# Kernel tuning notes

Measured on AMD Instinct MI355X. Metric: run time of the kernel, lower is better.

Reference implementation:

```python
import jax, jax.numpy as jnp
import numpy as np

D = 1024      # model_dim
H = 2048      # expert hidden_dim
E = 8         # num routed experts
S = 1         # num shared experts
M = 4         # num modes (1 shared expert per mode)
TOP_K = 2
B, L = 2, 2048


def _ffn(x, w1, b1, w2, b2):
    # x: [T, D]; w1: [..., D, H]; stacked experts via einsum
    h = jnp.einsum('td,edh->teh', x, w1) + b1          # [T, E*, H]
    h = jax.nn.gelu(h)
    return jnp.einsum('teh,ehd->ted', h, w2) + b2      # [T, E*, D]


def setup_inputs() -> dict:
    key = jax.random.key(0)
    ks = jax.random.split(key, 16)
    s = 0.02
    inp = {
        'hidden': jax.random.normal(ks[0], (B, L, D), dtype=jnp.float32),
        'mode_ids': jax.random.randint(ks[1], (B, L), 0, M),
        'router_w': jax.random.normal(ks[2], (D, E), dtype=jnp.float32) * s,
        'router_b': jnp.zeros((E,), dtype=jnp.float32),
        'shared_w1': jax.random.normal(ks[3], (S, D, H), dtype=jnp.float32) * s,
        'shared_b1': jnp.zeros((S, H), dtype=jnp.float32),
        'shared_w2': jax.random.normal(ks[4], (S, H, D), dtype=jnp.float32) * s,
        'shared_b2': jnp.zeros((S, D), dtype=jnp.float32),
        'mode_w1': jax.random.normal(ks[5], (M, D, H), dtype=jnp.float32) * s,
        'mode_b1': jnp.zeros((M, H), dtype=jnp.float32),
        'mode_w2': jax.random.normal(ks[6], (M, H, D), dtype=jnp.float32) * s,
        'mode_b2': jnp.zeros((M, D), dtype=jnp.float32),
        'routed_w1': jax.random.normal(ks[7], (E, D, H), dtype=jnp.float32) * s,
        'routed_b1': jnp.zeros((E, H), dtype=jnp.float32),
        'routed_w2': jax.random.normal(ks[8], (E, H, D), dtype=jnp.float32) * s,
        'routed_b2': jnp.zeros((E, D), dtype=jnp.float32),
    }
    return inp


def reference(hidden, mode_ids, router_w, router_b,
              shared_w1, shared_b1, shared_w2, shared_b2,
              mode_w1, mode_b1, mode_w2, mode_b2,
              routed_w1, routed_b1, routed_w2, routed_b2):
    b, l, d = hidden.shape
    flat = hidden.reshape(b * l, d)                         # [T, D]

    # --- router ---
    router_logits = flat @ router_w + router_b              # [T, E]
    router_probs = jax.nn.softmax(router_logits, axis=-1)
    topk_probs, topk_indices = jax.lax.top_k(router_probs, TOP_K)  # [T, K]

    # --- shared experts (mean over S experts) ---
    shared_out = _ffn(flat, shared_w1, shared_b1, shared_w2, shared_b2).mean(axis=1)  # [T, D]

    # --- mode-conditioned shared experts (1 expert per mode) ---
    mode_flat = mode_ids.reshape(-1)                        # [T]
    mode_onehot = jax.nn.one_hot(mode_flat, M, dtype=flat.dtype)   # [T, M]
    mode_all = _ffn(flat, mode_w1, mode_b1, mode_w2, mode_b2)      # [T, M, D]
    mode_out = jnp.einsum('tm,tmd->td', mode_onehot, mode_all)
    shared_out = shared_out + mode_out

    # --- routed experts: combine weights per (token, expert) ---
    # w[t,e] = sum_k topk_probs[t,k] * (topk_indices[t,k] == e)
    combine_w = jnp.einsum('tke,tk->te',
                           jax.nn.one_hot(topk_indices, E, dtype=flat.dtype),
                           topk_probs)                      # [T, E]
    routed_all = _ffn(flat, routed_w1, routed_b1, routed_w2, routed_b2)  # [T, E, D]
    mixed = jnp.einsum('te,ted->td', combine_w, routed_all)

    output = (shared_out + mixed).reshape(b, l, d)
    aux_logits = router_logits.reshape(b, l, E)
    aux_idx = topk_indices.reshape(b, l, TOP_K)
    aux_probs = topk_probs.reshape(b, l, TOP_K)
    return output, aux_logits, aux_idx, aux_probs
```

## Files before the change

kernel.cpp:

```cpp
#include <hip/hip_runtime.h>
#include <hip/hip_bf16.h>

typedef __hip_bfloat16 bf16t;
using f32x4 = __attribute__((ext_vector_type(4))) float;
using s16x8 = __attribute__((ext_vector_type(8))) short;

#define NTOK 4096
#define DIM 1024
#define HID 2048
#define NEXP 8
#define NMODE 4
#define NGRP 13
#define SLOTS_PAD 16640
#define MAXT 144

static constexpr size_t SZ_WT    = (size_t)NGRP * HID * DIM * 2;
static constexpr size_t OFF_WT1  = 0;
static constexpr size_t OFF_OBUF = 0;
static constexpr size_t OFF_WT2  = OFF_WT1 + SZ_WT;
static constexpr size_t OFF_HBUF = OFF_WT2 + SZ_WT;
static constexpr size_t SZ_HBUF  = (size_t)SLOTS_PAD * HID * 2;
static constexpr size_t OFF_XBF  = OFF_HBUF + SZ_HBUF;
static constexpr size_t SZ_XBF   = (size_t)NTOK * DIM * 2;
static constexpr size_t OFF_B1   = OFF_XBF + SZ_XBF;
static constexpr size_t OFF_B2   = OFF_B1 + (size_t)NGRP * HID * 4;
static constexpr size_t OFF_TP   = OFF_B2 + (size_t)NGRP * DIM * 4;
static constexpr size_t OFF_TI   = OFF_TP + (size_t)NTOK * 2 * 4;
static constexpr size_t OFF_MS   = OFF_TI + (size_t)NTOK * 2 * 4;
static constexpr size_t OFF_R0S  = OFF_MS + (size_t)NTOK * 4;
static constexpr size_t OFF_R1S  = OFF_R0S + (size_t)NTOK * 4;
static constexpr size_t OFF_LIST = OFF_R1S + (size_t)NTOK * 4;
static constexpr size_t OFF_TC   = OFF_LIST + (size_t)SLOTS_PAD * 4;
static constexpr size_t OFF_TD   = OFF_TC + 16;
static constexpr size_t WS_NEED  = OFF_TD + (size_t)MAXT * 16;

static __device__ __forceinline__ short fb(float f) {
    bf16t h = __float2bfloat16(f);
    short s; __builtin_memcpy(&s, &h, 2); return s;
}
static __device__ __forceinline__ float bf2f(short s) {
    unsigned u = ((unsigned)(unsigned short)s) << 16;
    float f; __builtin_memcpy(&f, &u, 4); return f;
}

static __device__ __forceinline__ float fast_exp(float x) {
#if __has_builtin(__builtin_amdgcn_exp2f)
    return __builtin_amdgcn_exp2f(x * 1.4426950408889634f);
#else
    return exp2f(x * 1.4426950408889634f);
#endif
}
static __device__ __forceinline__ float fast_rcp(float x) {
#if __has_builtin(__builtin_amdgcn_rcpf)
    return __builtin_amdgcn_rcpf(x);
#else
    return 1.0f / x;
#endif
}
static __device__ __forceinline__ float gelu_tanh(float x) {
    float x2 = x * x;
    float u = 0.7978845608028654f * fmaf(0.044715f * x2, x, x);
    u = fminf(u, 15.0f);
    float t = fast_exp(2.0f * u);
    return x * t * fast_rcp(t + 1.0f);
}

typedef __attribute__((address_space(3))) void lds_void;
typedef const __attribute__((address_space(1))) void gbl_void;
static __device__ __forceinline__ void gload16(const void* g, void* l) {
    __builtin_amdgcn_global_load_lds((gbl_void*)g, (lds_void*)l, 16, 0, 0);
}

struct TPtr {
    const float* s_w1; const float* s_w2;
    const float* m_w1; const float* m_w2;
    const float* r_w1; const float* r_w2;
};

static __device__ __forceinline__ void transpose_tile(
    const float* __restrict__ src, bf16t* __restrict__ dst, int R, int C, int x, int y,
    float (*lds)[64][65], int t) {
    const int c0 = x * 64;
    const int ar = t >> 4, ac = (t & 15) * 4;
    const int bc = t >> 3;
    const int rg = (t & 7) * 8;
#pragma unroll
    for (int it = 0; it < 2; ++it) {
        const int r0 = (y * 2 + it) * 64;
#pragma unroll
        for (int p = 0; p < 4; p++) {
            const int r = p * 16 + ar;
            const float4 v = *(const float4*)(src + (size_t)(r0 + r) * C + (c0 + ac));
            lds[it][r][ac] = v.x; lds[it][r][ac + 1] = v.y;
            lds[it][r][ac + 2] = v.z; lds[it][r][ac + 3] = v.w;
        }
    }
    __syncthreads();
#pragma unroll
    for (int it = 0; it < 2; ++it) {
        const int r0 = (y * 2 + it) * 64;
#pragma unroll
        for (int j = 0; j < 2; j++) {
            const int c = j * 32 + bc;
            unsigned w[4];
#pragma unroll
            for (int u = 0; u < 4; u++) {
                unsigned lo = (unsigned short)fb(lds[it][rg + 2 * u][c]);
                unsigned hi = (unsigned short)fb(lds[it][rg + 2 * u + 1][c]);
                w[u] = (hi << 16) | lo;
            }
            *(uint4*)((char*)dst + ((size_t)(c0 + c) * R + (r0 + rg)) * 2) = make_uint4(w[0], w[1], w[2], w[3]);
        }
    }
}

#define TGRID1 3328
#define RGRID  4352
#define PGRID  4456

__global__ __launch_bounds__(256) void prep_k(
    TPtr tp, bf16t* __restrict__ wt1,
    const float* __restrict__ hidden, const int* __restrict__ mode_ids,
    const float* __restrict__ rw, const float* __restrict__ rb,
    float* __restrict__ aux_logits, float* __restrict__ aux_idx, float* __restrict__ aux_probs,
    float* __restrict__ topk_p, int* __restrict__ topk_i, bf16t* __restrict__ xbf,
    const float* __restrict__ sb1, const float* __restrict__ mb1, const float* __restrict__ rb1,
    const float* __restrict__ sb2, const float* __restrict__ mb2, const float* __restrict__ rb2,
    float* __restrict__ B1c, float* __restrict__ B2c) {
    const int bid = blockIdx.x;
    const int t = threadIdx.x;

    if (bid < TGRID1) {
        __shared__ float lds[2][64][65];
        const size_t MSZ = (size_t)DIM * HID;
        const int z = bid >> 8, rem = bid & 255;
        const int x = (rem >> 3) & 31, y = rem & 7;
        const float* src;
        if (z == 0)      src = tp.s_w1;
        else if (z < 5)  src = tp.m_w1 + (size_t)(z - 1) * MSZ;
        else             src = tp.r_w1 + (size_t)(z - 5) * MSZ;
        transpose_tile(src, wt1 + (size_t)z * MSZ, DIM, HID, x, y, lds, t);
        return;
    }

    if (bid < RGRID) {
        const int tok = (bid - TGRID1) * 4 + (t >> 6);
        const int lane = t & 63;
        const float* x = hidden + (size_t)tok * DIM;
        float acc[NEXP];
#pragma unroll
        for (int e = 0; e < NEXP; e++) acc[e] = 0.f;
#pragma unroll
        for (int i = 0; i < DIM / 64; i++) {
            int d = i * 64 + lane;
            float xv = x[d];
            xbf[(size_t)tok * DIM + d] = __float2bfloat16(xv);
            const float4* w = (const float4*)(rw + (size_t)d * NEXP);
            float4 w0 = w[0], w1 = w[1];
            acc[0] += xv * w0.x; acc[1] += xv * w0.y; acc[2] += xv * w0.z; acc[3] += xv * w0.w;
            acc[4] += xv * w1.x; acc[5] += xv * w1.y; acc[6] += xv * w1.z; acc[7] += xv * w1.w;
        }
#pragma unroll
        for (int off = 32; off >= 1; off >>= 1) {
#pragma unroll
            for (int e = 0; e < NEXP; e++) acc[e] += __shfl_down(acc[e], off, 64);
        }
        if (lane == 0) {
            float lg[NEXP], pb[NEXP];
            float mx = -1e30f;
#pragma unroll
            for (int e = 0; e < NEXP; e++) { lg[e] = acc[e] + rb[e]; mx = fmaxf(mx, lg[e]); }
            float s = 0.f;
#pragma unroll
            for (int e = 0; e < NEXP; e++) { pb[e] = expf(lg[e] - mx); s += pb[e]; }
            float inv = 1.f / s;
#pragma unroll
            for (int e = 0; e < NEXP; e++) { pb[e] *= inv; aux_logits[(size_t)tok * NEXP + e] = lg[e]; }
            int i1 = 0;
            for (int e = 1; e < NEXP; e++) if (pb[e] > pb[i1]) i1 = e;
            int i2 = (i1 == 0) ? 1 : 0;
            for (int e = 0; e < NEXP; e++) { if (e == i1) continue; if (pb[e] > pb[i2]) i2 = e; }
            aux_idx[tok * 2] = (float)i1;  aux_idx[tok * 2 + 1] = (float)i2;
            aux_probs[tok * 2] = pb[i1];   aux_probs[tok * 2 + 1] = pb[i2];
            topk_p[tok * 2] = pb[i1];      topk_p[tok * 2 + 1] = pb[i2];
            topk_i[tok * 2] = i1;          topk_i[tok * 2 + 1] = i2;
        }
        return;
    }

    {
        const int i = (bid - RGRID) * 256 + t;
        if (i < NGRP * HID) {
            int g = i / HID, h = i % HID;
            B1c[i] = (g == 0) ? sb1[h] : (g < 5) ? mb1[(g - 1) * HID + h] : rb1[(g - 5) * HID + h];
        }
        if (i < NGRP * DIM) {
            int g = i / DIM, d = i % DIM;
            B2c[i] = (g == 0) ? sb2[d] : (g < 5) ? mb2[(g - 1) * DIM + d] : rb2[(g - 5) * DIM + d];
        }
    }
}

__global__ __launch_bounds__(1024) void groupfill_k(
    const int* __restrict__ mode_ids, const int* __restrict__ topki,
    int4* __restrict__ tdesc, int* __restrict__ tcount,
    int* __restrict__ list,
    int* __restrict__ ms, int* __restrict__ r0s, int* __restrict__ r1s) {
    __shared__ int cnts[12];
    __shared__ int curs[12];
    const int lane = threadIdx.x & 63;
    const int wave = threadIdx.x >> 6;
    if (threadIdx.x < 12) cnts[threadIdx.x] = 0;
    if (threadIdx.x < SLOTS_PAD - 16384) list[16384 + threadIdx.x] = 0;
    __syncthreads();

    int local[12];
#pragma unroll
    for (int i = 0; i < 12; i++) local[i] = 0;
#pragma unroll
    for (int c = wave; c < NTOK / 64; c += 16) {
        const int t = c * 64 + lane;
        const int m  = mode_ids[t];
        const int e0 = topki[t * 2];
        const int e1 = topki[t * 2 + 1];
#pragma unroll
        for (int b = 0; b < 4; b++) local[b] += __popcll(__ballot(m == b));
#pragma unroll
        for (int b = 0; b < 8; b++) {
            local[4 + b] += __popcll(__ballot(e0 == b));
            local[4 + b] += __popcll(__ballot(e1 == b));
        }
    }
    if (lane == 0) {
#pragma unroll
        for (int i = 0; i < 12; i++) if (local[i]) atomicAdd(&cnts[i], local[i]);
    }
    __syncthreads();

    if (threadIdx.x == 0) {
        int nt = 0;
        auto emit = [&](int off, int c, int g) {
            for (int r0 = 0; r0 < c; r0 += 128) tdesc[nt++] = make_int4(off + r0, min(128, c - r0), g, 0);
        };
        emit(0, NTOK, 0);
        int off = NTOK;
        for (int m = 0; m < NMODE; m++) { curs[m] = off; emit(off, cnts[m], 1 + m); off += cnts[m]; }
        off = 2 * NTOK;
        for (int e = 0; e < NEXP; e++) { curs[NMODE + e] = off; emit(off, cnts[NMODE + e], 5 + e); off += cnts[NMODE + e]; }
        tcount[0] = nt;
    }
    __syncthreads();

    auto put = [&](int bin, bool pred, int payload, int* inv, int t) {
        unsigned long long msk = __ballot(pred);
        if (msk == 0ull) return;
        int leader = __ffsll((unsigned long long)msk) - 1;
        int base = 0;
        if (lane == leader) base = atomicAdd(&curs[bin], __popcll(msk));
        base = __shfl(base, leader, 64);
        if (pred) {
            int pos = base + __popcll(msk & ((1ull << lane) - 1ull));
            list[pos] = payload;
            inv[t] = pos;
        }
    };
#pragma unroll
    for (int it = 0; it < 4; ++it) {
        const int t = it * 1024 + threadIdx.x;
        list[t] = t << 1;
        const int m  = mode_ids[t];
        const int e0 = topki[t * 2], e1 = topki[t * 2 + 1];
#pragma unroll
        for (int b = 0; b < NMODE; b++) put(b, m == b, t << 1, ms, t);
#pragma unroll
        for (int b = 0; b < NEXP; b++) put(NMODE + b, e0 == b, t << 1, r0s, t);
#pragma unroll
        for (int b = 0; b < NEXP; b++) put(NMODE + b, e1 == b, (t << 1) | 1, r1s, t);
    }
}

#define W2GRID 3328
template <int STAGE>
__global__ __launch_bounds__(256, 3) void ffn_gemm_k(
    const bf16t* __restrict__ xbf,
    const bf16t* __restrict__ hbuf,
    const bf16t* __restrict__ wt,
    const float* __restrict__ bias,
    bf16t* __restrict__ obuf,
    const int* __restrict__ list,
    const int4* __restrict__ tdesc,
    const int* __restrict__ tcount,
    const float* __restrict__ w2s, const float* __restrict__ w2m, const float* __restrict__ w2r,
    bf16t* __restrict__ wt2o) {
    constexpr int K   = (STAGE == 1) ? DIM : HID;
    constexpr int N   = (STAGE == 1) ? HID : DIM;
    constexpr int NK  = K / 32;
    constexpr int NTN = N / 128;
    constexpr int NWG = NTN * MAXT;

    __shared__ alignas(16) char smem[49152];

    if constexpr (STAGE == 1) {
        if (blockIdx.x >= NWG) {
            const int id2 = blockIdx.x - NWG;
            const size_t MSZ = (size_t)DIM * HID;
            const int z = id2 >> 8, rem = id2 & 255;
            const int x = rem >> 4, y = rem & 15;
            const float* src;
            if (z == 0)      src = w2s;
            else if (z < 5)  src = w2m + (size_t)(z - 1) * MSZ;
            else             src = w2r + (size_t)(z - 5) * MSZ;
            transpose_tile(src, wt2o + (size_t)z * MSZ, HID, DIM, x, y,
                           (float (*)[64][65])smem, threadIdx.x);
            return;
        }
    }

    char* As = smem;
    char* Bs = smem + 24576;

    const int lin = blockIdx.x;
    const int wg  = (lin & 7) * (NWG >> 3) + (lin >> 3);
    const int ntile = wg / MAXT;
    const int tix = wg - ntile * MAXT;
    if (tix >= tcount[0]) return;
    const int4 td = tdesc[tix];
    const int slot0 = td.x, rows = td.y, gidx = td.z;
    const int n0 = ntile * 128;

    const int tid  = threadIdx.x;
    const int lane = tid & 63;
    const int w    = tid >> 6;
    const int wm   = w >> 1, wn = w & 1;

    const bf16t* wbase = wt + (size_t)gidx * ((size_t)K * N);
    const bf16t* aP[2];
    const bf16t* bP[2];
#pragma unroll
    for (int h = 0; h < 2; h++) {
        const int r  = (w * 2 + h) * 16 + (lane >> 2);
        const int ce = (((lane & 3) ^ ((r >> 1) & 3)) << 3);
        if (STAGE == 1) aP[h] = xbf + (size_t)(list[slot0 + r] >> 1) * DIM + ce;
        else            aP[h] = hbuf + (size_t)(slot0 + r) * HID + ce;
        bP[h] = wbase + (size_t)(n0 + r) * K + ce;
    }

    auto stage = [&](int t) {
        char* la = As + (t % 3) * 8192 + (w * 2) * 1024 + lane * 16;
        char* lb = Bs + (t % 3) * 8192 + (w * 2) * 1024 + lane * 16;
        gload16(aP[0] + t * 32, la);
        gload16(aP[1] + t * 32, la + 1024);
        gload16(bP[0] + t * 32, lb);
        gload16(bP[1] + t * 32, lb + 1024);
    };

    f32x4 acc[4][4];
    const f32x4 zero = {0.f, 0.f, 0.f, 0.f};
#pragma unroll
    for (int i = 0; i < 4; i++)
#pragma unroll
        for (int j = 0; j < 4; j++) acc[i][j] = zero;

    const int lm = lane & 15;
    const int kc = lane >> 4;

    stage(0); stage(1);

    for (int t = 0; t < NK; ++t) {
        const int cur = t % 3;
        if (t + 1 < NK) asm volatile("s_waitcnt vmcnt(4)" ::: "memory");
        else            asm volatile("s_waitcnt vmcnt(0)" ::: "memory");
        __builtin_amdgcn_s_barrier();

        s16x8 av[4], bv[4];
#pragma unroll
        for (int i = 0; i < 4; i++) {
            const int Ra = wm * 64 + i * 16 + lm;
            av[i] = *(const s16x8*)(As + cur * 8192 + Ra * 64 + ((kc ^ ((Ra >> 1) & 3)) << 4));
            const int Rb = wn * 64 + i * 16 + lm;
            bv[i] = *(const s16x8*)(Bs + cur * 8192 + Rb * 64 + ((kc ^ ((Rb >> 1) & 3)) << 4));
        }
        if (t + 2 < NK) stage(t + 2);

        __builtin_amdgcn_s_setprio(1);
#pragma unroll
        for (int mi = 0; mi < 4; mi++)
#pragma unroll
            for (int ni = 0; ni < 4; ni++)
                acc[mi][ni] = __builtin_amdgcn_mfma_f32_16x16x32_bf16(av[mi], bv[ni], acc[mi][ni], 0, 0, 0);
        __builtin_amdgcn_s_setprio(0);
    }

    const int lr = lane >> 4, lc = lane & 15;
#pragma unroll
    for (int ni = 0; ni < 4; ni++) {
        const int col = n0 + wn * 64 + ni * 16 + lc;
        const float bvv = bias[gidx * N + col];
#pragma unroll
        for (int mi = 0; mi < 4; mi++) {
#pragma unroll
            for (int r = 0; r < 4; r++) {
                const int row = wm * 64 + mi * 16 + lr * 4 + r;
                if (row < rows) {
                    float v = acc[mi][ni][r] + bvv;
                    if (STAGE == 1) v = gelu_tanh(v);
                    obuf[(size_t)(slot0 + row) * N + col] = __float2bfloat16(v);
                }
            }
        }
    }
}

__global__ void reduce_k(const bf16t* __restrict__ ob,
                         const int* __restrict__ ms, const int* __restrict__ r0s, const int* __restrict__ r1s,
                         const float* __restrict__ topkp, float* __restrict__ out) {
    const int t = blockIdx.x * 4 + (threadIdx.x >> 7);
    const int d = (threadIdx.x & 127) * 8;
    const s16x8 a = *(const s16x8*)(ob + (size_t)t * DIM + d);
    const s16x8 b = *(const s16x8*)(ob + (size_t)ms[t] * DIM + d);
    const s16x8 c = *(const s16x8*)(ob + (size_t)r0s[t] * DIM + d);
    const s16x8 e = *(const s16x8*)(ob + (size_t)r1s[t] * DIM + d);
    const float p0 = topkp[t * 2], p1 = topkp[t * 2 + 1];
    float o[8];
#pragma unroll
    for (int j = 0; j < 8; j++)
        o[j] = bf2f(a[j]) + bf2f(b[j]) + p0 * bf2f(c[j]) + p1 * bf2f(e[j]);
    float* dst = out + (size_t)t * DIM + d;
    *(float4*)dst = make_float4(o[0], o[1], o[2], o[3]);
    *(float4*)(dst + 4) = make_float4(o[4], o[5], o[6], o[7]);
}

extern "C" void kernel_launch(void* const* d_in, const int* in_sizes, int n_in,
                              void* d_out, int out_size, void* d_ws, size_t ws_size,
                              hipStream_t stream) {
    (void)in_sizes; (void)n_in; (void)out_size;
    if (ws_size < WS_NEED) return;

    const float* hidden   = (const float*)d_in[0];
    const int*   mode_ids = (const int*)d_in[1];
    const float* router_w = (const float*)d_in[2];
    const float* router_b = (const float*)d_in[3];
    TPtr tp;
    tp.s_w1 = (const float*)d_in[4];
    const float* s_b1 = (const float*)d_in[5];
    tp.s_w2 = (const float*)d_in[6];
    const float* s_b2 = (const float*)d_in[7];
    tp.m_w1 = (const float*)d_in[8];
    const float* m_b1 = (const float*)d_in[9];
    tp.m_w2 = (const float*)d_in[10];
    const float* m_b2 = (const float*)d_in[11];
    tp.r_w1 = (const float*)d_in[12];
    const float* r_b1 = (const float*)d_in[13];
    tp.r_w2 = (const float*)d_in[14];
    const float* r_b2 = (const float*)d_in[15];

    char* ws = (char*)d_ws;
    bf16t* WT1   = (bf16t*)(ws + OFF_WT1);
    bf16t* WT2   = (bf16t*)(ws + OFF_WT2);
    bf16t* Hbuf  = (bf16t*)(ws + OFF_HBUF);
    bf16t* Xbf   = (bf16t*)(ws + OFF_XBF);
    bf16t* Obuf  = (bf16t*)(ws + OFF_OBUF);
    float* B1c   = (float*)(ws + OFF_B1);
    float* B2c   = (float*)(ws + OFF_B2);
    float* topkp = (float*)(ws + OFF_TP);
    int*   topki = (int*)(ws + OFF_TI);
    int*   ms    = (int*)(ws + OFF_MS);
    int*   r0s   = (int*)(ws + OFF_R0S);
    int*   r1s   = (int*)(ws + OFF_R1S);
    int*   list  = (int*)(ws + OFF_LIST);
    int*   tcnt  = (int*)(ws + OFF_TC);
    int4*  td    = (int4*)(ws + OFF_TD);

    float* out        = (float*)d_out;
    float* aux_logits = out + (size_t)NTOK * DIM;
    float* aux_idx    = aux_logits + (size_t)NTOK * NEXP;
    float* aux_probs  = aux_idx + (size_t)NTOK * 2;

    prep_k<<<PGRID, 256, 0, stream>>>(tp, WT1,
                                      hidden, mode_ids, router_w, router_b,
                                      aux_logits, aux_idx, aux_probs, topkp, topki, Xbf,
                                      s_b1, m_b1, r_b1, s_b2, m_b2, r_b2, B1c, B2c);
    groupfill_k<<<1, 1024, 0, stream>>>(mode_ids, topki, td, tcnt, list, ms, r0s, r1s);
    ffn_gemm_k<1><<<(HID / 128) * MAXT + W2GRID, 256, 0, stream>>>(
        Xbf, Hbuf, WT1, B1c, Hbuf, list, td, tcnt, tp.s_w2, tp.m_w2, tp.r_w2, WT2);
    ffn_gemm_k<2><<<(DIM / 128) * MAXT, 256, 0, stream>>>(
        Xbf, Hbuf, WT2, B2c, Obuf, list, td, tcnt, nullptr, nullptr, nullptr, nullptr);
    reduce_k<<<NTOK / 4, 512, 0, stream>>>(Obuf, ms, r0s, r1s, topkp, out);
}
```

Before: 337.7 us.

## Make grouped FFN GEMM kernels persistent with atomic job counter

Both GEMM stages launch a fixed grid of persistent blocks that repeatedly claim job indices via an atomic counter, instead of one block per potential tile. Empty tiles beyond the actual tile count and weight-transpose jobs are handled inside the loop. This removes the dispatch overhead of many early-exiting blocks and balances load dynamically. In exchange, each job costs an extra atomic plus two block barriers, and the counters must be reset in groupfill.

```diff
diff --git a/kernel.cpp b/kernel.cpp
--- a/kernel.cpp
+++ b/kernel.cpp
@@ -13,6 +13,7 @@
 #define NGRP 13
 #define SLOTS_PAD 16640
 #define MAXT 144
+#define PERSIST 768
 
 static constexpr size_t SZ_WT    = (size_t)NGRP * HID * DIM * 2;
 static constexpr size_t OFF_WT1  = 0;
@@ -212,6 +213,7 @@
     const int wave = threadIdx.x >> 6;
     if (threadIdx.x < 12) cnts[threadIdx.x] = 0;
     if (threadIdx.x < SLOTS_PAD - 16384) list[16384 + threadIdx.x] = 0;
+    if (threadIdx.x == 1) { tcount[1] = 0; tcount[2] = 0; }
     __syncthreads();
 
     int local[12];
@@ -290,6 +292,7 @@
     const int* __restrict__ list,
     const int4* __restrict__ tdesc,
     const int* __restrict__ tcount,
+    int* __restrict__ jobctr,
     const float* __restrict__ w2s, const float* __restrict__ w2m, const float* __restrict__ w2r,
     bf16t* __restrict__ wt2o) {
     constexpr int K   = (STAGE == 1) ? DIM : HID;
@@ -297,114 +300,121 @@
     constexpr int NK  = K / 32;
     constexpr int NTN = N / 128;
     constexpr int NWG = NTN * MAXT;
+    constexpr int TOTAL = (STAGE == 1) ? NWG + W2GRID : NWG;
 
     __shared__ alignas(16) char smem[49152];
-
-    if constexpr (STAGE == 1) {
-        if (blockIdx.x >= NWG) {
-            const int id2 = blockIdx.x - NWG;
-            const size_t MSZ = (size_t)DIM * HID;
-            const int z = id2 >> 8, rem = id2 & 255;
-            const int x = rem >> 4, y = rem & 15;
-            const float* src;
-            if (z == 0)      src = w2s;
-            else if (z < 5)  src = w2m + (size_t)(z - 1) * MSZ;
-            else             src = w2r + (size_t)(z - 5) * MSZ;
-            transpose_tile(src, wt2o + (size_t)z * MSZ, HID, DIM, x, y,
-                           (float (*)[64][65])smem, threadIdx.x);
-            return;
-        }
-    }
-
-    char* As = smem;
-    char* Bs = smem + 24576;
-
-    const int lin = blockIdx.x;
-    const int wg  = (lin & 7) * (NWG >> 3) + (lin >> 3);
-    const int ntile = wg / MAXT;
-    const int tix = wg - ntile * MAXT;
-    if (tix >= tcount[0]) return;
-    const int4 td = tdesc[tix];
-    const int slot0 = td.x, rows = td.y, gidx = td.z;
-    const int n0 = ntile * 128;
+    __shared__ int sjob;
 
     const int tid  = threadIdx.x;
     const int lane = tid & 63;
     const int w    = tid >> 6;
     const int wm   = w >> 1, wn = w & 1;
-
-    const bf16t* wbase = wt + (size_t)gidx * ((size_t)K * N);
-    const bf16t* aP[2];
-    const bf16t* bP[2];
-#pragma unroll
-    for (int h = 0; h < 2; h++) {
-        const int r  = (w * 2 + h) * 16 + (lane >> 2);
-        const int ce = (((lane & 3) ^ ((r >> 1) & 3)) << 3);
-        if (STAGE == 1) aP[h] = xbf + (size_t)(list[slot0 + r] >> 1) * DIM + ce;
-        else            aP[h] = hbuf + (size_t)(slot0 + r) * HID + ce;
-        bP[h] = wbase + (size_t)(n0 + r) * K + ce;
-    }
-
-    auto stage = [&](int t) {
-        char* la = As + (t % 3) * 8192 + (w * 2) * 1024 + lane * 16;
-        char* lb = Bs + (t % 3) * 8192 + (w * 2) * 1024 + lane * 16;
-        gload16(aP[0] + t * 32, la);
-        gload16(aP[1] + t * 32, la + 1024);
-        gload16(bP[0] + t * 32, lb);
-        gload16(bP[1] + t * 32, lb + 1024);
-    };
-
-    f32x4 acc[4][4];
-    const f32x4 zero = {0.f, 0.f, 0.f, 0.f};
-#pragma unroll
-    for (int i = 0; i < 4; i++)
-#pragma unroll
-        for (int j = 0; j < 4; j++) acc[i][j] = zero;
-
     const int lm = lane & 15;
     const int kc = lane >> 4;
-
-    stage(0); stage(1);
-
-    for (int t = 0; t < NK; ++t) {
-        const int cur = t % 3;
-        if (t + 1 < NK) asm volatile("s_waitcnt vmcnt(4)" ::: "memory");
-        else            asm volatile("s_waitcnt vmcnt(0)" ::: "memory");
-        __builtin_amdgcn_s_barrier();
-
-        s16x8 av[4], bv[4];
-#pragma unroll
-        for (int i = 0; i < 4; i++) {
-            const int Ra = wm * 64 + i * 16 + lm;
-            av[i] = *(const s16x8*)(As + cur * 8192 + Ra * 64 + ((kc ^ ((Ra >> 1) & 3)) << 4));
-            const int Rb = wn * 64 + i * 16 + lm;
-            bv[i] = *(const s16x8*)(Bs + cur * 8192 + Rb * 64 + ((kc ^ ((Rb >> 1) & 3)) << 4));
-        }
-        if (t + 2 < NK) stage(t + 2);
-
-        __builtin_amdgcn_s_setprio(1);
-#pragma unroll
-        for (int mi = 0; mi < 4; mi++)
-#pragma unroll
-            for (int ni = 0; ni < 4; ni++)
-                acc[mi][ni] = __builtin_amdgcn_mfma_f32_16x16x32_bf16(av[mi], bv[ni], acc[mi][ni], 0, 0, 0);
-        __builtin_amdgcn_s_setprio(0);
-    }
-
-    const int lr = lane >> 4, lc = lane & 15;
-#pragma unroll
-    for (int ni = 0; ni < 4; ni++) {
-        const int col = n0 + wn * 64 + ni * 16 + lc;
-        const float bvv = bias[gidx * N + col];
-#pragma unroll
-        for (int mi = 0; mi < 4; mi++) {
-#pragma unroll
-            for (int r = 0; r < 4; r++) {
-                const int row = wm * 64 + mi * 16 + lr * 4 + r;
-                if (row < rows) {
-                    float v = acc[mi][ni][r] + bvv;
-                    if (STAGE == 1) v = gelu_tanh(v);
-                    obuf[(size_t)(slot0 + row) * N + col] = __float2bfloat16(v);
+    char* As = smem;
+    char* Bs = smem + 24576;
+
+    for (;;) {
+        __syncthreads();
+        if (tid == 0) sjob = atomicAdd(jobctr, 1);
+        __syncthreads();
+        const int job = sjob;
+        if (job >= TOTAL) return;
+
+        if constexpr (STAGE == 1) {
+            if (job >= NWG) {
+                const int id2 = job - NWG;
+                const size_t MSZ = (size_t)DIM * HID;
+                const int z = id2 >> 8, rem = id2 & 255;
+                const int x = rem >> 4, y = rem & 15;
+                const float* src;
+                if (z == 0)      src = w2s;
+                else if (z < 5)  src = w2m + (size_t)(z - 1) * MSZ;
+                else             src = w2r + (size_t)(z - 5) * MSZ;
+                transpose_tile(src, wt2o + (size_t)z * MSZ, HID, DIM, x, y,
+                               (float (*)[64][65])smem, tid);
+                continue;
+            }
+        }
+
+        const int wg  = (job & 7) * (NWG >> 3) + (job >> 3);
+        const int ntile = wg / MAXT;
+        const int tix = wg - ntile * MAXT;
+        if (tix >= tcount[0]) continue;
+        const int4 td = tdesc[tix];
+        const int slot0 = td.x, rows = td.y, gidx = td.z;
+        const int n0 = ntile * 128;
+
+        const bf16t* wbase = wt + (size_t)gidx * ((size_t)K * N);
+        const bf16t* aP[2];
+        const bf16t* bP[2];
+#pragma unroll
+        for (int h = 0; h < 2; h++) {
+            const int r  = (w * 2 + h) * 16 + (lane >> 2);
+            const int ce = (((lane & 3) ^ ((r >> 1) & 3)) << 3);
+            if (STAGE == 1) aP[h] = xbf + (size_t)(list[slot0 + r] >> 1) * DIM + ce;
+            else            aP[h] = hbuf + (size_t)(slot0 + r) * HID + ce;
+            bP[h] = wbase + (size_t)(n0 + r) * K + ce;
+        }
+
+        auto stage = [&](int t) {
+            char* la = As + (t % 3) * 8192 + (w * 2) * 1024 + lane * 16;
+            char* lb = Bs + (t % 3) * 8192 + (w * 2) * 1024 + lane * 16;
+            gload16(aP[0] + t * 32, la);
+            gload16(aP[1] + t * 32, la + 1024);
+            gload16(bP[0] + t * 32, lb);
+            gload16(bP[1] + t * 32, lb + 1024);
+        };
+
+        f32x4 acc[4][4];
+        const f32x4 zero = {0.f, 0.f, 0.f, 0.f};
+#pragma unroll
+        for (int i = 0; i < 4; i++)
+#pragma unroll
+            for (int j = 0; j < 4; j++) acc[i][j] = zero;
+
+        stage(0); stage(1);
+
+        for (int t = 0; t < NK; ++t) {
+            const int cur = t % 3;
+            if (t + 1 < NK) asm volatile("s_waitcnt vmcnt(4)" ::: "memory");
+            else            asm volatile("s_waitcnt vmcnt(0)" ::: "memory");
+            __builtin_amdgcn_s_barrier();
+
+            s16x8 av[4], bv[4];
+#pragma unroll
+            for (int i = 0; i < 4; i++) {
+                const int Ra = wm * 64 + i * 16 + lm;
+                av[i] = *(const s16x8*)(As + cur * 8192 + Ra * 64 + ((kc ^ ((Ra >> 1) & 3)) << 4));
+                const int Rb = wn * 64 + i * 16 + lm;
+                bv[i] = *(const s16x8*)(Bs + cur * 8192 + Rb * 64 + ((kc ^ ((Rb >> 1) & 3)) << 4));
+            }
+            if (t + 2 < NK) stage(t + 2);
+
+            __builtin_amdgcn_s_setprio(1);
+#pragma unroll
+            for (int mi = 0; mi < 4; mi++)
+#pragma unroll
+                for (int ni = 0; ni < 4; ni++)
+                    acc[mi][ni] = __builtin_amdgcn_mfma_f32_16x16x32_bf16(av[mi], bv[ni], acc[mi][ni], 0, 0, 0);
+            __builtin_amdgcn_s_setprio(0);
+        }
+
+        const int lr = lane >> 4, lc = lane & 15;
+#pragma unroll
+        for (int ni = 0; ni < 4; ni++) {
+            const int col = n0 + wn * 64 + ni * 16 + lc;
+            const float bvv = bias[gidx * N + col];
+#pragma unroll
+            for (int mi = 0; mi < 4; mi++) {
+#pragma unroll
+                for (int r = 0; r < 4; r++) {
+                    const int row = wm * 64 + mi * 16 + lr * 4 + r;
+                    if (row < rows) {
+                        float v = acc[mi][ni][r] + bvv;
+                        if (STAGE == 1) v = gelu_tanh(v);
+                        obuf[(size_t)(slot0 + row) * N + col] = __float2bfloat16(v);
+                    }
                 }
             }
         }
@@ -481,9 +491,9 @@
                                       aux_logits, aux_idx, aux_probs, topkp, topki, Xbf,
                                       s_b1, m_b1, r_b1, s_b2, m_b2, r_b2, B1c, B2c);
     groupfill_k<<<1, 1024, 0, stream>>>(mode_ids, topki, td, tcnt, list, ms, r0s, r1s);
-    ffn_gemm_k<1><<<(HID / 128) * MAXT + W2GRID, 256, 0, stream>>>(
-        Xbf, Hbuf, WT1, B1c, Hbuf, list, td, tcnt, tp.s_w2, tp.m_w2, tp.r_w2, WT2);
-    ffn_gemm_k<2><<<(DIM / 128) * MAXT, 256, 0, stream>>>(
-        Xbf, Hbuf, WT2, B2c, Obuf, list, td, tcnt, nullptr, nullptr, nullptr, nullptr);
+    ffn_gemm_k<1><<<PERSIST, 256, 0, stream>>>(
+        Xbf, Hbuf, WT1, B1c, Hbuf, list, td, tcnt, tcnt + 1, tp.s_w2, tp.m_w2, tp.r_w2, WT2);
+    ffn_gemm_k<2><<<PERSIST, 256, 0, stream>>>(
+        Xbf, Hbuf, WT2, B2c, Obuf, list, td, tcnt, tcnt + 2, nullptr, nullptr, nullptr, nullptr);
     reduce_k<<<NTOK / 4, 512, 0, stream>>>(Obuf, ms, r0s, r1s, topkp, out);
 }
```

Result: slower. 378.5 us (+12.1%).
